# Performance work log

Hardware: AMD Instinct MI355X
Metric: run time of the kernel (lower is better)

The kernel has to match this reference:

```python
import jax, jax.numpy as jnp
import numpy as np

OUT, IN, GROUP = 8192, 8192, 128  # meta.shape=(out,in), group_size over out dim


def unpack_int4(packed, out_shape):
    """Unpack uint8 bytes (two nibbles each) into signed int8 in [-8,7].
    Matches torch: inter[0::2]=lo, inter[1::2]=hi."""
    flat = packed.reshape(-1)
    lo = (flat & 15).astype(jnp.int8)
    hi = ((flat >> 4) & 15).astype(jnp.int8)
    lo = jnp.where(lo >= 8, lo - 16, lo)
    hi = jnp.where(hi >= 8, hi - 16, hi)
    inter = jnp.stack([lo, hi], axis=-1).reshape(-1)  # interleave lo/hi
    total = out_shape[0] * out_shape[1]
    return inter[:total].reshape(out_shape)


def setup_inputs() -> dict:
    key = jax.random.key(0)
    kx, kq, ks, kb = jax.random.split(key, 4)
    x = jax.random.normal(kx, (16, IN), dtype=jnp.float32)
    # packed int4 weights: one byte holds two nibbles -> OUT*IN/2 bytes
    q_packed = jax.random.randint(kq, (OUT * IN // 2,), 0, 256, dtype=jnp.int32).astype(jnp.uint8)
    # per-group scales (group over out dim), positive small values
    scale = jax.random.uniform(ks, (OUT // GROUP,), dtype=jnp.float32) * 0.01 + 1e-4
    bias = jax.random.normal(kb, (OUT,), dtype=jnp.float32) * 0.01
    return {"x": x, "q_packed": q_packed, "scale": scale, "bias": bias}


def reference(x, q_packed, scale, bias):
    # unpack + per-group dequant, then matmul (CPU fallback path of QuantLinear.forward)
    q_int = unpack_int4(q_packed, (OUT, IN)).astype(jnp.float32)  # (OUT, IN)
    s = jnp.repeat(scale, GROUP)[:, None]                         # (OUT, 1) expanded scales
    W = s * q_int                                                 # dequantized fp weight
    return x @ W.T + bias                                         # (B, OUT)
```

## Files before the change

kernel.cpp:

```cpp
#include <hip/hip_runtime.h>
#include <hip/hip_bf16.h>

#define OUT_N 8192
#define IN_N  8192
#define QROW  (IN_N / 2)
#define NCH   8
#define CH32  64

typedef __attribute__((ext_vector_type(8))) short short8v;
typedef __attribute__((ext_vector_type(4))) float f32x4;

__device__ __forceinline__ unsigned int bf16pk(float a, float b) {
    __hip_bfloat162 h = __float22bfloat162_rn(make_float2(a, b));
    unsigned int u;
    __builtin_memcpy(&u, &h, 4);
    return u;
}

__device__ __forceinline__ void gld_lds16(const int* gsrc, int* ldst_base) {
    __builtin_amdgcn_global_load_lds(
        (const __attribute__((address_space(1))) void*)gsrc,
        (__attribute__((address_space(3))) void*)ldst_base, 16, 0, 0);
}

__global__ __launch_bounds__(256) void xconv_kernel(
    const float* __restrict__ x, unsigned short* __restrict__ xb)
{
    int i = (blockIdx.x * 256 + threadIdx.x) * 4;
    float4 v = *(const float4*)(x + i);
    uint2 u = { bf16pk(v.x, v.y), bf16pk(v.z, v.w) };
    *(uint2*)(xb + i) = u;
}

__global__ __launch_bounds__(512, 4) void qlin_mfma_kernel(
    const int*            __restrict__ qp,
    const unsigned short* __restrict__ xb,
    const float*          __restrict__ scale,
    const float*          __restrict__ bias,
    float*                __restrict__ out)
{
    __shared__ int   qbuf[8][2][16 * CH32];
    __shared__ float red[8][16][17];

    const int t = threadIdx.x;
    const int w = t >> 6;
    const int l = t & 63;
    const int g = l >> 4;
    const int r = l & 15;
    const int tile = blockIdx.x;
    const int obase = tile * 16;

    const int* qwbase = qp + (size_t)obase * QROW + w * (QROW / 8);
    const int drow = l >> 4;
    const unsigned short* xwbase = xb + (size_t)r * IN_N + w * (IN_N / 8);

    f32x4 acc = {0.f, 0.f, 0.f, 0.f};
    uint4 xr[2][4];

    #pragma unroll
    for (int s = 0; s < 4; ++s)
        xr[0][s] = *(const uint4*)(xwbase + s * 32 + g * 8);
    #pragma unroll
    for (int p = 0; p < 4; ++p) {
        const int row = 4 * p + drow;
        const int j   = (l & 15) ^ (row & 15);
        gld_lds16(qwbase + (size_t)row * QROW + j * 4, &qbuf[w][0][p * 256]);
    }

    #pragma unroll
    for (int c = 0; c < NCH; ++c) {
        const int cur = c & 1;

        if (c + 1 < NCH) {
            #pragma unroll
            for (int s = 0; s < 4; ++s)
                xr[cur ^ 1][s] = *(const uint4*)(xwbase + (c + 1) * 128 + s * 32 + g * 8);
            #pragma unroll
            for (int p = 0; p < 4; ++p) {
                const int row = 4 * p + drow;
                const int j   = (l & 15) ^ (row & 15);
                gld_lds16(qwbase + (size_t)row * QROW + (c + 1) * CH32 + j * 4,
                          &qbuf[w][cur ^ 1][p * 256]);
            }
            asm volatile("s_waitcnt vmcnt(8)" ::: "memory");
        } else {
            asm volatile("s_waitcnt vmcnt(0)" ::: "memory");
        }
        __builtin_amdgcn_sched_barrier(0);

        const char* wb = (const char*)qbuf[w][cur];
        #pragma unroll
        for (int s = 0; s < 4; ++s) {
            const int4 q = *(const int4*)(wb + r * 256 + ((((s << 2) + g) ^ r) << 4));
            uint4 ub = {
                bf16pk((float)((q.x << 28) >> 28), (float)((q.x << 24) >> 28)),
                bf16pk((float)((q.y << 28) >> 28), (float)((q.y << 24) >> 28)),
                bf16pk((float)((q.z << 28) >> 28), (float)((q.z << 24) >> 28)),
                bf16pk((float)((q.w << 28) >> 28), (float)((q.w << 24) >> 28))
            };
            short8v bfrag = __builtin_bit_cast(short8v, ub);
            short8v afrag = __builtin_bit_cast(short8v, xr[cur][s]);
            acc = __builtin_amdgcn_mfma_f32_16x16x32_bf16(afrag, bfrag, acc, 0, 0, 0);
        }
    }

    red[w][g * 4 + 0][r] = acc[0];
    red[w][g * 4 + 1][r] = acc[1];
    red[w][g * 4 + 2][r] = acc[2];
    red[w][g * 4 + 3][r] = acc[3];
    __syncthreads();

    if (t < 256) {
        const int b = t >> 4;
        const int o = t & 15;
        const int oc = obase + o;
        float v = 0.f;
        #pragma unroll
        for (int i = 0; i < 8; ++i) v += red[i][b][o];
        out[b * OUT_N + oc] = v * scale[oc >> 7] + bias[oc];
    }
}

extern "C" void kernel_launch(void* const* d_in, const int* in_sizes, int n_in,
                              void* d_out, int out_size, void* d_ws, size_t ws_size,
                              hipStream_t stream) {
    (void)in_sizes; (void)n_in; (void)ws_size; (void)out_size;
    const float* x     = (const float*)d_in[0];
    const int*   qp    = (const int*)d_in[1];
    const float* scale = (const float*)d_in[2];
    const float* bias  = (const float*)d_in[3];
    float*       out   = (float*)d_out;
    unsigned short* xb = (unsigned short*)d_ws;

    xconv_kernel<<<dim3((16 * IN_N) / (256 * 4)), dim3(256), 0, stream>>>(x, xb);
    qlin_mfma_kernel<<<dim3(OUT_N / 16), dim3(512), 0, stream>>>(qp, xb, scale, bias, out);
}
```

Measured before the change: 32.86 us.

## Stage weight chunks block-wide with row-per-wave loads and two-chunk prefetch

Each wave previously loaded and consumed only its own narrow K-slice of all 16 weight rows. Now each wave loads 2 full rows of a large 512-int chunk into one shared double buffer, so global reads become long contiguous row segments. The main loop prefetches two chunks ahead, waits on vmcnt, and uses block-wide s_barriers so that all waves can read rows loaded by others. The intent is better coalescing and more bytes in flight per request; the cost is two extra barriers per chunk and coupling between waves.

Result: slower. 42.03 us (+27.9%).

```diff
diff --git a/kernel.cpp b/kernel.cpp
--- a/kernel.cpp
+++ b/kernel.cpp
@@ -5,7 +5,7 @@
 #define IN_N  8192
 #define QROW  (IN_N / 2)
 #define NCH   8
-#define CH32  64
+#define CH32  512
 
 typedef __attribute__((ext_vector_type(8))) short short8v;
 typedef __attribute__((ext_vector_type(4))) float f32x4;
@@ -23,6 +23,11 @@
         (__attribute__((address_space(3))) void*)ldst_base, 16, 0, 0);
 }
 
+#define SBAR()   asm volatile("s_barrier" ::: "memory")
+#define VMCNT8() asm volatile("s_waitcnt vmcnt(8)" ::: "memory")
+#define VMCNT0() asm volatile("s_waitcnt vmcnt(0)" ::: "memory")
+#define SCHED0() __builtin_amdgcn_sched_barrier(0)
+
 __global__ __launch_bounds__(256) void xconv_kernel(
     const float* __restrict__ x, unsigned short* __restrict__ xb)
 {
@@ -39,7 +44,7 @@
     const float*          __restrict__ bias,
     float*                __restrict__ out)
 {
-    __shared__ int   qbuf[8][2][16 * CH32];
+    __shared__ int   qbuf[2][16][CH32];
     __shared__ float red[8][16][17];
 
     const int t = threadIdx.x;
@@ -50,48 +55,44 @@
     const int tile = blockIdx.x;
     const int obase = tile * 16;
 
-    const int* qwbase = qp + (size_t)obase * QROW + w * (QROW / 8);
-    const int drow = l >> 4;
-    const unsigned short* xwbase = xb + (size_t)r * IN_N + w * (IN_N / 8);
+    const int R0 = 2 * w;
+    const int* qr0 = qp + (size_t)(obase + R0) * QROW;
+    const int* qr1 = qr0 + QROW;
+    const int sw0 = (l ^ (R0 & 15)) * 4;
+    const int sw1 = (l ^ ((R0 + 1) & 15)) * 4;
+    const unsigned short* xbase = xb + (size_t)r * IN_N + w * 128 + g * 8;
 
     f32x4 acc = {0.f, 0.f, 0.f, 0.f};
     uint4 xr[2][4];
 
-    #pragma unroll
-    for (int s = 0; s < 4; ++s)
-        xr[0][s] = *(const uint4*)(xwbase + s * 32 + g * 8);
-    #pragma unroll
-    for (int p = 0; p < 4; ++p) {
-        const int row = 4 * p + drow;
-        const int j   = (l & 15) ^ (row & 15);
-        gld_lds16(qwbase + (size_t)row * QROW + j * 4, &qbuf[w][0][p * 256]);
-    }
+#define ISSUE(c_, slot_)                                                      \
+    do {                                                                      \
+        _Pragma("unroll")                                                     \
+        for (int s = 0; s < 4; ++s)                                           \
+            xr[slot_][s] = *(const uint4*)(xbase + (c_) * 1024 + s * 32);     \
+        gld_lds16(qr0 + (c_) * CH32 + sw0,       &qbuf[(c_) & 1][R0][0]);     \
+        gld_lds16(qr0 + (c_) * CH32 + 256 + sw0, &qbuf[(c_) & 1][R0][256]);   \
+        gld_lds16(qr1 + (c_) * CH32 + sw1,       &qbuf[(c_) & 1][R0 + 1][0]); \
+        gld_lds16(qr1 + (c_) * CH32 + 256 + sw1, &qbuf[(c_) & 1][R0 + 1][256]);\
+    } while (0)
+
+    ISSUE(0, 0);
+    ISSUE(1, 1);
 
     #pragma unroll
     for (int c = 0; c < NCH; ++c) {
-        const int cur = c & 1;
+        if (c < NCH - 1) VMCNT8();
+        else             VMCNT0();
+        SCHED0();
+        SBAR();
+        SCHED0();
 
-        if (c + 1 < NCH) {
-            #pragma unroll
-            for (int s = 0; s < 4; ++s)
-                xr[cur ^ 1][s] = *(const uint4*)(xwbase + (c + 1) * 128 + s * 32 + g * 8);
-            #pragma unroll
-            for (int p = 0; p < 4; ++p) {
-                const int row = 4 * p + drow;
-                const int j   = (l & 15) ^ (row & 15);
-                gld_lds16(qwbase + (size_t)row * QROW + (c + 1) * CH32 + j * 4,
-                          &qbuf[w][cur ^ 1][p * 256]);
-            }
-            asm volatile("s_waitcnt vmcnt(8)" ::: "memory");
-        } else {
-            asm volatile("s_waitcnt vmcnt(0)" ::: "memory");
-        }
-        __builtin_amdgcn_sched_barrier(0);
-
-        const char* wb = (const char*)qbuf[w][cur];
+        const char* bufb = (const char*)&qbuf[c & 1][0][0];
         #pragma unroll
         for (int s = 0; s < 4; ++s) {
-            const int4 q = *(const int4*)(wb + r * 256 + ((((s << 2) + g) ^ r) << 4));
+            const int j0   = w * 16 + s * 4 + g;
+            const int slot = (j0 & 64) | ((j0 & 63) ^ r);
+            const int4 q = *(const int4*)(bufb + r * 2048 + slot * 16);
             uint4 ub = {
                 bf16pk((float)((q.x << 28) >> 28), (float)((q.x << 24) >> 28)),
                 bf16pk((float)((q.y << 28) >> 28), (float)((q.y << 24) >> 28)),
@@ -99,10 +100,16 @@
                 bf16pk((float)((q.w << 28) >> 28), (float)((q.w << 24) >> 28))
             };
             short8v bfrag = __builtin_bit_cast(short8v, ub);
-            short8v afrag = __builtin_bit_cast(short8v, xr[cur][s]);
+            short8v afrag = __builtin_bit_cast(short8v, xr[c & 1][s]);
             acc = __builtin_amdgcn_mfma_f32_16x16x32_bf16(afrag, bfrag, acc, 0, 0, 0);
         }
+
+        SCHED0();
+        SBAR();
+        SCHED0();
+        if (c + 2 < NCH) ISSUE(c + 2, c & 1);
     }
+#undef ISSUE
 
     red[w][g * 4 + 0][r] = acc[0];
     red[w][g * 4 + 1][r] = acc[1];
```

## Use four waves per block with larger per-wave K chunks

Applied to the files above, without the earlier changes.

Cuts the block from 8 to 4 waves. Each wave now covers twice the K range, using 128-int chunks, 8 MFMA steps per chunk and 8 outstanding loads per stage. The LDS swizzle is adjusted to an 8-way XOR, and the cross-wave reduction now sums 4 partials. The aim is more memory-level parallelism per wave and less reduction overhead. The cost is more registers for the doubled x prefetch buffers and lower launch-bound occupancy.

Result: slower. 36.66 us (+11.5%).

```diff
diff --git a/kernel.cpp b/kernel.cpp
--- a/kernel.cpp
+++ b/kernel.cpp
@@ -4,8 +4,11 @@
 #define OUT_N 8192
 #define IN_N  8192
 #define QROW  (IN_N / 2)
+#define WAVES 4
+#define KPW   (IN_N / WAVES)
 #define NCH   8
-#define CH32  64
+#define CH32  128
+#define STEPS 8
 
 typedef __attribute__((ext_vector_type(8))) short short8v;
 typedef __attribute__((ext_vector_type(4))) float f32x4;
@@ -23,6 +26,8 @@
         (__attribute__((address_space(3))) void*)ldst_base, 16, 0, 0);
 }
 
+#define SCHED0() __builtin_amdgcn_sched_barrier(0)
+
 __global__ __launch_bounds__(256) void xconv_kernel(
     const float* __restrict__ x, unsigned short* __restrict__ xb)
 {
@@ -32,15 +37,15 @@
     *(uint2*)(xb + i) = u;
 }
 
-__global__ __launch_bounds__(512, 4) void qlin_mfma_kernel(
+__global__ __launch_bounds__(256, 2) void qlin_mfma_kernel(
     const int*            __restrict__ qp,
     const unsigned short* __restrict__ xb,
     const float*          __restrict__ scale,
     const float*          __restrict__ bias,
     float*                __restrict__ out)
 {
-    __shared__ int   qbuf[8][2][16 * CH32];
-    __shared__ float red[8][16][17];
+    __shared__ int   qbuf[WAVES][2][16 * CH32];
+    __shared__ float red[WAVES][16][17];
 
     const int t = threadIdx.x;
     const int w = t >> 6;
@@ -50,48 +55,49 @@
     const int tile = blockIdx.x;
     const int obase = tile * 16;
 
-    const int* qwbase = qp + (size_t)obase * QROW + w * (QROW / 8);
-    const int drow = l >> 4;
-    const unsigned short* xwbase = xb + (size_t)r * IN_N + w * (IN_N / 8);
+    const int* qwbase = qp + (size_t)obase * QROW + w * (KPW / 2);
+    const int dR = l >> 5;
+    const int dslot = l & 31;
+    const unsigned short* xwbase = xb + (size_t)r * IN_N + w * KPW + g * 8;
 
     f32x4 acc = {0.f, 0.f, 0.f, 0.f};
-    uint4 xr[2][4];
+    uint4 xr[2][STEPS];
 
-    #pragma unroll
-    for (int s = 0; s < 4; ++s)
-        xr[0][s] = *(const uint4*)(xwbase + s * 32 + g * 8);
-    #pragma unroll
-    for (int p = 0; p < 4; ++p) {
-        const int row = 4 * p + drow;
-        const int j   = (l & 15) ^ (row & 15);
-        gld_lds16(qwbase + (size_t)row * QROW + j * 4, &qbuf[w][0][p * 256]);
-    }
+#define ISSUE_Q(c_)                                                         \
+    do { _Pragma("unroll")                                                  \
+        for (int p = 0; p < 8; ++p) {                                       \
+            const int R = 2 * p + dR;                                       \
+            const int s_ = dslot ^ (R & 7);    \
+            gld_lds16(qwbase + (size_t)R * QROW + (c_) * CH32 + s_ * 4,     \
+                      &qbuf[w][(c_) & 1][(2 * p) * CH32]);                  \
+        } } while (0)
+
+#define ISSUE_X(c_)                                                         \
+    do { _Pragma("unroll")                                                  \
+        for (int s = 0; s < STEPS; ++s)                                     \
+            xr[(c_) & 1][s] = *(const uint4*)(xwbase + (c_) * 256 + s * 32);\
+        } while (0)
+
+    ISSUE_X(0);
+    ISSUE_Q(0);
 
     #pragma unroll
     for (int c = 0; c < NCH; ++c) {
         const int cur = c & 1;
 
         if (c + 1 < NCH) {
-            #pragma unroll
-            for (int s = 0; s < 4; ++s)
-                xr[cur ^ 1][s] = *(const uint4*)(xwbase + (c + 1) * 128 + s * 32 + g * 8);
-            #pragma unroll
-            for (int p = 0; p < 4; ++p) {
-                const int row = 4 * p + drow;
-                const int j   = (l & 15) ^ (row & 15);
-                gld_lds16(qwbase + (size_t)row * QROW + (c + 1) * CH32 + j * 4,
-                          &qbuf[w][cur ^ 1][p * 256]);
-            }
-            asm volatile("s_waitcnt vmcnt(8)" ::: "memory");
+            ISSUE_X(c + 1);
+            ISSUE_Q(c + 1);
+            asm volatile("s_waitcnt vmcnt(16)" ::: "memory");
         } else {
             asm volatile("s_waitcnt vmcnt(0)" ::: "memory");
         }
-        __builtin_amdgcn_sched_barrier(0);
+        SCHED0();
 
-        const char* wb = (const char*)qbuf[w][cur];
+        const char* wb = (const char*)&qbuf[w][cur][0];
         #pragma unroll
-        for (int s = 0; s < 4; ++s) {
-            const int4 q = *(const int4*)(wb + r * 256 + ((((s << 2) + g) ^ r) << 4));
+        for (int s = 0; s < STEPS; ++s) {
+            const int4 q = *(const int4*)(wb + r * 512 + ((((s << 2) + g) ^ (r & 7)) << 4));
             uint4 ub = {
                 bf16pk((float)((q.x << 28) >> 28), (float)((q.x << 24) >> 28)),
                 bf16pk((float)((q.y << 28) >> 28), (float)((q.y << 24) >> 28)),
@@ -103,6 +109,8 @@
             acc = __builtin_amdgcn_mfma_f32_16x16x32_bf16(afrag, bfrag, acc, 0, 0, 0);
         }
     }
+#undef ISSUE_Q
+#undef ISSUE_X
 
     red[w][g * 4 + 0][r] = acc[0];
     red[w][g * 4 + 1][r] = acc[1];
@@ -110,13 +118,13 @@
     red[w][g * 4 + 3][r] = acc[3];
     __syncthreads();
 
-    if (t < 256) {
+    {
         const int b = t >> 4;
         const int o = t & 15;
         const int oc = obase + o;
         float v = 0.f;
         #pragma unroll
-        for (int i = 0; i < 8; ++i) v += red[i][b][o];
+        for (int i = 0; i < WAVES; ++i) v += red[i][b][o];
         out[b * OUT_N + oc] = v * scale[oc >> 7] + bias[oc];
     }
 }
@@ -133,5 +141,5 @@
     unsigned short* xb = (unsigned short*)d_ws;
 
     xconv_kernel<<<dim3((16 * IN_N) / (256 * 4)), dim3(256), 0, stream>>>(x, xb);
-    qlin_mfma_kernel<<<dim3(OUT_N / 16), dim3(512), 0, stream>>>(qp, xb, scale, bias, out);
+    qlin_mfma_kernel<<<dim3(OUT_N / 16), dim3(256), 0, stream>>>(qp, xb, scale, bias, out);
 }
```

## Replace double-buffered pipeline with larger single-buffered chunks per wave

Applied to the files above, without the earlier changes.

Drops the LDS double buffering and software prefetch. Each wave now loads 128-int chunks (twice as wide) into a single buffer, waits for all loads, then computes eight MFMA steps per chunk, with a new XOR swizzle over 8 rows. This halves the loop iterations and keeps LDS use the same, but the loads of the next chunk no longer overlap the current chunk's compute. The added sched_barrier keeps the next iteration's loads from being hoisted above the compute.

Measured after the change: 33.55 us. +2.1%, slower.

```diff
diff --git a/kernel.cpp b/kernel.cpp
--- a/kernel.cpp
+++ b/kernel.cpp
@@ -4,8 +4,9 @@
 #define OUT_N 8192
 #define IN_N  8192
 #define QROW  (IN_N / 2)
-#define NCH   8
-#define CH32  64
+#define NCH   4
+#define CH32  128
+#define STEPS 8
 
 typedef __attribute__((ext_vector_type(8))) short short8v;
 typedef __attribute__((ext_vector_type(4))) float f32x4;
@@ -39,7 +40,7 @@
     const float*          __restrict__ bias,
     float*                __restrict__ out)
 {
-    __shared__ int   qbuf[8][2][16 * CH32];
+    __shared__ int   qbuf[8][16][CH32];
     __shared__ float red[8][16][17];
 
     const int t = threadIdx.x;
@@ -51,47 +52,33 @@
     const int obase = tile * 16;
 
     const int* qwbase = qp + (size_t)obase * QROW + w * (QROW / 8);
-    const int drow = l >> 4;
-    const unsigned short* xwbase = xb + (size_t)r * IN_N + w * (IN_N / 8);
+    const int dR   = l >> 5;
+    const int dsl  = l & 31;
+    const unsigned short* xwbase = xb + (size_t)r * IN_N + w * (IN_N / 8) + g * 8;
 
     f32x4 acc = {0.f, 0.f, 0.f, 0.f};
-    uint4 xr[2][4];
-
-    #pragma unroll
-    for (int s = 0; s < 4; ++s)
-        xr[0][s] = *(const uint4*)(xwbase + s * 32 + g * 8);
-    #pragma unroll
-    for (int p = 0; p < 4; ++p) {
-        const int row = 4 * p + drow;
-        const int j   = (l & 15) ^ (row & 15);
-        gld_lds16(qwbase + (size_t)row * QROW + j * 4, &qbuf[w][0][p * 256]);
-    }
+    uint4 xr[STEPS];
 
     #pragma unroll
     for (int c = 0; c < NCH; ++c) {
-        const int cur = c & 1;
+        #pragma unroll
+        for (int p = 0; p < 8; ++p) {
+            const int R = 2 * p + dR;
+            const int j = dsl ^ ((R & 7) << 2);
+            gld_lds16(qwbase + (size_t)R * QROW + c * CH32 + j * 4,
+                      &qbuf[w][2 * p][0]);
+        }
+        #pragma unroll
+        for (int s = 0; s < STEPS; ++s)
+            xr[s] = *(const uint4*)(xwbase + c * 256 + s * 32);
 
-        if (c + 1 < NCH) {
-            #pragma unroll
-            for (int s = 0; s < 4; ++s)
-                xr[cur ^ 1][s] = *(const uint4*)(xwbase + (c + 1) * 128 + s * 32 + g * 8);
-            #pragma unroll
-            for (int p = 0; p < 4; ++p) {
-                const int row = 4 * p + drow;
-                const int j   = (l & 15) ^ (row & 15);
-                gld_lds16(qwbase + (size_t)row * QROW + (c + 1) * CH32 + j * 4,
-                          &qbuf[w][cur ^ 1][p * 256]);
-            }
-            asm volatile("s_waitcnt vmcnt(8)" ::: "memory");
-        } else {
-            asm volatile("s_waitcnt vmcnt(0)" ::: "memory");
-        }
+        asm volatile("s_waitcnt vmcnt(0)" ::: "memory");
         __builtin_amdgcn_sched_barrier(0);
 
-        const char* wb = (const char*)qbuf[w][cur];
+        const char* wb = (const char*)&qbuf[w][0][0];
         #pragma unroll
-        for (int s = 0; s < 4; ++s) {
-            const int4 q = *(const int4*)(wb + r * 256 + ((((s << 2) + g) ^ r) << 4));
+        for (int s = 0; s < STEPS; ++s) {
+            const int4 q = *(const int4*)(wb + r * 512 + ((((s << 2) + g) ^ ((r & 7) << 2)) << 4));
             uint4 ub = {
                 bf16pk((float)((q.x << 28) >> 28), (float)((q.x << 24) >> 28)),
                 bf16pk((float)((q.y << 28) >> 28), (float)((q.y << 24) >> 28)),
@@ -99,9 +86,10 @@
                 bf16pk((float)((q.w << 28) >> 28), (float)((q.w << 24) >> 28))
             };
             short8v bfrag = __builtin_bit_cast(short8v, ub);
-            short8v afrag = __builtin_bit_cast(short8v, xr[cur][s]);
+            short8v afrag = __builtin_bit_cast(short8v, xr[s]);
             acc = __builtin_amdgcn_mfma_f32_16x16x32_bf16(afrag, bfrag, acc, 0, 0, 0);
         }
+        __builtin_amdgcn_sched_barrier(0);
     }
 
     red[w][g * 4 + 0][r] = acc[0];
```
